# Kernel tuning notes

Measured on AMD Instinct MI355X. Metric: run time of the kernel, lower is better.

The kernel has to match this reference:

```python
import jax, jax.numpy as jnp
import numpy as np

B, T, C = 4, 2048, 1024
H = 16
D = C // H  # head_dim = 64


def setup_inputs() -> dict:
    key = jax.random.key(0)
    ks = jax.random.split(key, 5)
    scale_in = 1.0 / np.sqrt(C)
    x = jax.random.normal(ks[0], (B, T, C), dtype=jnp.float32)
    w_qkv = jax.random.normal(ks[1], (C, 3 * C), dtype=jnp.float32) * scale_in
    b_qkv = jnp.zeros((3 * C,), dtype=jnp.float32)
    w_proj = jax.random.normal(ks[2], (C, C), dtype=jnp.float32) * scale_in
    b_proj = jnp.zeros((C,), dtype=jnp.float32)
    return {"x": x, "w_qkv": w_qkv, "b_qkv": b_qkv, "w_proj": w_proj, "b_proj": b_proj}


def reference(x, w_qkv, b_qkv, w_proj, b_proj):
    # fused QKV projection: [B,T,3C]
    qkv = x @ w_qkv + b_qkv
    q, k, v = jnp.split(qkv, 3, axis=-1)
    # [B,T,C] -> [B,H,T,D]
    q = q.reshape(B, T, H, D).transpose(0, 2, 1, 3)
    k = k.reshape(B, T, H, D).transpose(0, 2, 1, 3)
    v = v.reshape(B, T, H, D).transpose(0, 2, 1, 3)
    scale = 1.0 / np.sqrt(D)
    scores = jnp.einsum('bhqd,bhkd->bhqk', q, k) * scale  # [B,H,T,T]
    causal = jnp.tril(jnp.ones((T, T), dtype=bool))
    scores = jnp.where(causal, scores, jnp.finfo(scores.dtype).min)
    attn = jax.nn.softmax(scores, axis=-1)
    y = jnp.einsum('bhqk,bhkd->bhqd', attn, v)  # [B,H,T,D]
    y = y.transpose(0, 2, 1, 3).reshape(B, T, C)
    return y @ w_proj + b_proj
```

## Files before the change

kernel.cpp:

```cpp
#include <hip/hip_runtime.h>

typedef unsigned short u16;
typedef unsigned int u32;
typedef unsigned long long u64;
typedef __attribute__((ext_vector_type(8))) short s16x8;
typedef __attribute__((ext_vector_type(4))) float f32x4;

#if __has_builtin(__builtin_amdgcn_exp2f)
#define EXP2(x) __builtin_amdgcn_exp2f(x)
#else
#define EXP2(x) __expf((x) * 0.69314718f)
#endif

#if __has_builtin(__builtin_amdgcn_rcpf)
#define RCP(x) __builtin_amdgcn_rcpf(x)
#else
#define RCP(x) (1.0f / (x))
#endif

#define GLL(gp, lp) __builtin_amdgcn_global_load_lds(                         \
    (const __attribute__((address_space(1))) unsigned int*)(const void*)(gp), \
    (__attribute__((address_space(3))) unsigned int*)(void*)(lp), 16, 0, 0)

__device__ __forceinline__ u16 f2bf(float f) {
    union { float f; u32 u; } v; v.f = f;
    u32 r = v.u + 0x7FFF + ((v.u >> 16) & 1);
    return (u16)(r >> 16);
}

__device__ __forceinline__ float bf2f(u16 b) {
    union { u32 u; float f; } v; v.u = ((u32)b) << 16;
    return v.f;
}

__device__ __forceinline__ s16x8 scale_frag(s16x8 v, float s) {
    s16x8 o;
#pragma unroll
    for (int i = 0; i < 8; i++) o[i] = (short)f2bf(bf2f((u16)v[i]) * s);
    return o;
}

__global__ __launch_bounds__(256) void cast_f32_bf16(const float* __restrict__ in,
                                                     u16* __restrict__ out) {
    size_t i = ((size_t)blockIdx.x * 256 + threadIdx.x) * 4;
    float4 f = *(const float4*)(in + i);
    u16 o[4] = { f2bf(f.x), f2bf(f.y), f2bf(f.z), f2bf(f.w) };
    *(unsigned long long*)(out + i) =
        (unsigned long long)o[0] | ((unsigned long long)o[1] << 16) |
        ((unsigned long long)o[2] << 32) | ((unsigned long long)o[3] << 48);
}

__global__ __launch_bounds__(256) void transpose_cast(const float* __restrict__ in,
                                                      u16* __restrict__ out,
                                                      int rows, int cols) {
    __shared__ float tile[32][33];
    int c0 = blockIdx.x * 32, r0 = blockIdx.y * 32;
    int tx = threadIdx.x, ty = threadIdx.y;
    for (int i = 0; i < 32; i += 8)
        tile[ty + i][tx] = in[(size_t)(r0 + ty + i) * cols + (c0 + tx)];
    __syncthreads();
    for (int i = 0; i < 32; i += 8)
        out[(size_t)(c0 + ty + i) * rows + (r0 + tx)] = f2bf(tile[tx][ty + i]);
}

template<int MODE>
__global__ __launch_bounds__(256, 3) void gemm_bt64(const u16* __restrict__ A,
                                                    const u16* __restrict__ BT,
                                                    const float* __restrict__ bias,
                                                    void* __restrict__ O1,
                                                    u16* __restrict__ vT,
                                                    int M, int N, int K) {
    __shared__ u16 As[128 * 64];
    __shared__ u16 Bs[128 * 64];
    int n0 = blockIdx.x * 128, m0 = blockIdx.y * 128;
    int tid = threadIdx.x, lane = tid & 63, w = tid >> 6;
    int row16 = lane & 15, quad = lane >> 4;
    int wm = (w >> 1) * 64, wn = (w & 1) * 64;
    f32x4 acc[4][4] = {};

    int lr = lane >> 3;
    int cswz = (lane & 7) ^ lr;
    const u16* Ag = A + (size_t)(m0 + w * 32 + lr) * K + cswz * 8;
    const u16* Bg = BT + (size_t)(n0 + w * 32 + lr) * K + cswz * 8;
    u16* Asl = As + (w * 32) * 64;
    u16* Bsl = Bs + (w * 32) * 64;

    for (int k0 = 0; k0 < K; k0 += 64) {
        __syncthreads();
#pragma unroll
        for (int j = 0; j < 4; j++) {
            GLL(Ag + k0 + (size_t)j * 8 * K, Asl + j * 8 * 64);
            GLL(Bg + k0 + (size_t)j * 8 * K, Bsl + j * 8 * 64);
        }
        __syncthreads();
#pragma unroll
        for (int kk = 0; kk < 2; kk++) {
            s16x8 af[4], bf[4];
#pragma unroll
            for (int mi = 0; mi < 4; mi++)
                af[mi] = *(const s16x8*)&As[(wm + mi * 16 + row16) * 64 +
                                            (((kk * 4 + quad) ^ (row16 & 7)) * 8)];
#pragma unroll
            for (int ni = 0; ni < 4; ni++)
                bf[ni] = *(const s16x8*)&Bs[(wn + ni * 16 + row16) * 64 +
                                            (((kk * 4 + quad) ^ (row16 & 7)) * 8)];
#pragma unroll
            for (int mi = 0; mi < 4; mi++)
#pragma unroll
                for (int ni = 0; ni < 4; ni++)
                    acc[mi][ni] = __builtin_amdgcn_mfma_f32_16x16x32_bf16(
                        af[mi], bf[ni], acc[mi][ni], 0, 0, 0);
        }
    }

#pragma unroll
    for (int ni = 0; ni < 4; ni++) {
        int col = n0 + wn + ni * 16 + row16;
        float bv = bias[col];
        if (MODE == 0) {
            float* O = (float*)O1;
#pragma unroll
            for (int mi = 0; mi < 4; mi++)
#pragma unroll
                for (int r = 0; r < 4; r++)
                    O[(size_t)(m0 + wm + mi * 16 + quad * 4 + r) * N + col] =
                        acc[mi][ni][r] + bv;
        } else {
            if (col < 2048) {
                u16* qk = (u16*)O1;
#pragma unroll
                for (int mi = 0; mi < 4; mi++)
#pragma unroll
                    for (int r = 0; r < 4; r++)
                        qk[(size_t)(m0 + wm + mi * 16 + quad * 4 + r) * 2048 + col] =
                            f2bf(acc[mi][ni][r] + bv);
            } else {
                int c = col - 2048;
#pragma unroll
                for (int mi = 0; mi < 4; mi++) {
                    int t0 = m0 + wm + mi * 16 + quad * 4;
                    int b = t0 >> 11;
                    u16 o0 = f2bf(acc[mi][ni][0] + bv);
                    u16 o1 = f2bf(acc[mi][ni][1] + bv);
                    u16 o2 = f2bf(acc[mi][ni][2] + bv);
                    u16 o3 = f2bf(acc[mi][ni][3] + bv);
                    u64 pack = (u64)o0 | ((u64)o1 << 16) | ((u64)o2 << 32) | ((u64)o3 << 48);
                    *(u64*)&vT[((size_t)(b * 1024) + c) * 2048 + (t0 & 2047)] = pack;
                }
            }
        }
    }
}

__global__ __launch_bounds__(256, 4) void attn_kernel(const u16* __restrict__ qk,
                                                      const u16* __restrict__ vT,
                                                      u16* __restrict__ y) {
    __shared__ u16 Kb[2][64 * 64];
    __shared__ u16 Vb[2][64 * 64];
    __shared__ u16 Ps[4 * 16 * 64];

    int tid = threadIdx.x, lane = tid & 63, w = tid >> 6;
    int row16 = lane & 15, quad = lane >> 4;
    int pairi = blockIdx.x;
    int bh = blockIdx.y;
    int b = bh >> 4, h = bh & 15;
    const u16* qkb = qk + (size_t)b * 2048 * 2048;
    const u16* vtb = vT + ((size_t)(b * 1024) + h * 64) * 2048;

    int lr = lane >> 3, cswz = (lane & 7) ^ lr;
    const u16* Kg = qkb + (size_t)(w * 16 + lr) * 2048 + 1024 + h * 64 + cswz * 8;
    const u16* Vg = vtb + (size_t)(w * 16 + lr) * 2048 + cswz * 8;
    u16* Psw = Ps + w * 1024;
    int sw = row16 & 7;

    s16x8 ones;
#pragma unroll
    for (int i = 0; i < 8; i++) ones[i] = (short)0x3F80;
    const float qs = 0.125f * 1.44269504f;

    for (int half = 0; half < 2; half++) {
        int qt = half ? pairi : (31 - pairi);
        int q0 = qt * 64;
        int niter = qt + 1;

        int qrow = q0 + w * 16 + row16;
        const u16* qp = qkb + (size_t)qrow * 2048 + h * 64 + quad * 8;
        s16x8 qf0 = scale_frag(*(const s16x8*)qp, qs);
        s16x8 qf1 = scale_frag(*(const s16x8*)(qp + 32), qs);

        f32x4 acc_o[4] = {};
        f32x4 acc_l = {};

        __syncthreads();
#pragma unroll
        for (int j = 0; j < 2; j++) {
            GLL(Kg + (size_t)j * 8 * 2048, Kb[0] + w * 16 * 64 + j * 8 * 64);
            GLL(Vg + (size_t)j * 8 * 2048, Vb[0] + w * 16 * 64 + j * 8 * 64);
        }

        for (int kb = 0; kb < niter; kb++) {
            int cur = kb & 1;
            __syncthreads();
            if (kb + 1 < niter) {
                int k1 = (kb + 1) * 64;
#pragma unroll
                for (int j = 0; j < 2; j++) {
                    GLL(Kg + (size_t)(k1 + j * 8) * 2048, Kb[cur ^ 1] + w * 16 * 64 + j * 8 * 64);
                    GLL(Vg + k1 + (size_t)j * 8 * 2048, Vb[cur ^ 1] + w * 16 * 64 + j * 8 * 64);
                }
            }
            const u16* Kc = Kb[cur];
            const u16* Vc = Vb[cur];
            int k0 = kb * 64;

            f32x4 s[4];
#pragma unroll
            for (int nk = 0; nk < 4; nk++) {
                s16x8 kf0 = *(const s16x8*)&Kc[(nk * 16 + row16) * 64 + ((quad ^ sw) * 8)];
                s16x8 kf1 = *(const s16x8*)&Kc[(nk * 16 + row16) * 64 + (((4 + quad) ^ sw) * 8)];
                f32x4 z = {};
                z = __builtin_amdgcn_mfma_f32_16x16x32_bf16(qf0, kf0, z, 0, 0, 0);
                z = __builtin_amdgcn_mfma_f32_16x16x32_bf16(qf1, kf1, z, 0, 0, 0);
                s[nk] = z;
            }
            if (kb == niter - 1) {
                int rowb = q0 + w * 16 + quad * 4;
#pragma unroll
                for (int nk = 0; nk < 4; nk++) {
                    int kj = k0 + nk * 16 + row16;
#pragma unroll
                    for (int r = 0; r < 4; r++)
                        if (kj > rowb + r) s[nk][r] = -__builtin_inff();
                }
            }
#pragma unroll
            for (int nk = 0; nk < 4; nk++)
#pragma unroll
                for (int r = 0; r < 4; r++) {
                    float p = EXP2(s[nk][r]);
                    int qr = quad * 4 + r;
                    Psw[qr * 64 + (((nk * 2 + (row16 >> 3)) ^ (qr & 7)) * 8) + (row16 & 7)] =
                        f2bf(p);
                }
#pragma unroll
            for (int kk = 0; kk < 2; kk++) {
                s16x8 pf = *(const s16x8*)&Psw[row16 * 64 + (((kk * 4 + quad) ^ sw) * 8)];
#pragma unroll
                for (int nd = 0; nd < 4; nd++) {
                    s16x8 vf = *(const s16x8*)&Vc[(nd * 16 + row16) * 64 +
                                                  (((kk * 4 + quad) ^ sw) * 8)];
                    acc_o[nd] = __builtin_amdgcn_mfma_f32_16x16x32_bf16(pf, vf, acc_o[nd], 0, 0, 0);
                }
                acc_l = __builtin_amdgcn_mfma_f32_16x16x32_bf16(pf, ones, acc_l, 0, 0, 0);
            }
        }

        int t0 = q0 + w * 16 + quad * 4;
#pragma unroll
        for (int r = 0; r < 4; r++) {
            float inv = RCP(acc_l[r]);
#pragma unroll
            for (int nd = 0; nd < 4; nd++)
                y[((size_t)b * 2048 + t0 + r) * 1024 + h * 64 + nd * 16 + row16] =
                    f2bf(acc_o[nd][r] * inv);
        }
    }
}

extern "C" void kernel_launch(void* const* d_in, const int* in_sizes, int n_in,
                              void* d_out, int out_size, void* d_ws, size_t ws_size,
                              hipStream_t stream) {
    const float* x      = (const float*)d_in[0];
    const float* w_qkv  = (const float*)d_in[1];
    const float* b_qkv  = (const float*)d_in[2];
    const float* w_proj = (const float*)d_in[3];
    const float* b_proj = (const float*)d_in[4];
    float* out = (float*)d_out;

    u16* ws     = (u16*)d_ws;
    u16* x_bf   = ws;
    u16* wqkvT  = x_bf  + (size_t)8192 * 1024;
    u16* wprojT = wqkvT + (size_t)3072 * 1024;
    u16* qkbuf  = wprojT + (size_t)1024 * 1024;
    u16* vT     = qkbuf + (size_t)8192 * 2048;
    u16* ybf    = vT    + (size_t)4096 * 2048;

    cast_f32_bf16<<<dim3(8192), dim3(256), 0, stream>>>(x, x_bf);
    transpose_cast<<<dim3(96, 32), dim3(32, 8), 0, stream>>>(w_qkv, wqkvT, 1024, 3072);
    transpose_cast<<<dim3(32, 32), dim3(32, 8), 0, stream>>>(w_proj, wprojT, 1024, 1024);
    gemm_bt64<1><<<dim3(24, 64), 256, 0, stream>>>(x_bf, wqkvT, b_qkv, (void*)qkbuf, vT, 8192, 3072, 1024);
    attn_kernel<<<dim3(16, 64), 256, 0, stream>>>(qkbuf, vT, ybf);
    gemm_bt64<0><<<dim3(8, 64), 256, 0, stream>>>(ybf, wprojT, b_proj, (void*)out, nullptr, 8192, 1024, 1024);
}
```

Measured before the change: 262.7 us.

## Stage V-transpose epilogue through LDS, remap attention blocks per XCD, truncate P

```diff
diff --git a/kernel.cpp b/kernel.cpp
--- a/kernel.cpp
+++ b/kernel.cpp
@@ -26,6 +26,11 @@
     union { float f; u32 u; } v; v.f = f;
     u32 r = v.u + 0x7FFF + ((v.u >> 16) & 1);
     return (u16)(r >> 16);
+}
+
+__device__ __forceinline__ u16 f2bf_trunc(float f) {
+    union { float f; u32 u; } v; v.f = f;
+    return (u16)(v.u >> 16);
 }
 
 __device__ __forceinline__ float bf2f(u16 b) {
@@ -64,14 +69,15 @@
 }
 
 template<int MODE>
-__global__ __launch_bounds__(256, 3) void gemm_bt64(const u16* __restrict__ A,
+__global__ __launch_bounds__(256, 4) void gemm_bt64(const u16* __restrict__ A,
                                                     const u16* __restrict__ BT,
                                                     const float* __restrict__ bias,
                                                     void* __restrict__ O1,
                                                     u16* __restrict__ vT,
                                                     int M, int N, int K) {
-    __shared__ u16 As[128 * 64];
-    __shared__ u16 Bs[128 * 64];
+    __shared__ u16 SMEM[18432];
+    u16* As = SMEM;
+    u16* Bs = SMEM + 8192;
     int n0 = blockIdx.x * 128, m0 = blockIdx.y * 128;
     int tid = threadIdx.x, lane = tid & 63, w = tid >> 6;
     int row16 = lane & 15, quad = lane >> 4;
@@ -113,41 +119,53 @@
         }
     }
 
-#pragma unroll
-    for (int ni = 0; ni < 4; ni++) {
-        int col = n0 + wn + ni * 16 + row16;
-        float bv = bias[col];
-        if (MODE == 0) {
-            float* O = (float*)O1;
+    if (MODE == 0) {
+        float* O = (float*)O1;
+#pragma unroll
+        for (int ni = 0; ni < 4; ni++) {
+            int col = n0 + wn + ni * 16 + row16;
+            float bv = bias[col];
 #pragma unroll
             for (int mi = 0; mi < 4; mi++)
 #pragma unroll
                 for (int r = 0; r < 4; r++)
                     O[(size_t)(m0 + wm + mi * 16 + quad * 4 + r) * N + col] =
                         acc[mi][ni][r] + bv;
-        } else {
-            if (col < 2048) {
-                u16* qk = (u16*)O1;
-#pragma unroll
-                for (int mi = 0; mi < 4; mi++)
-#pragma unroll
-                    for (int r = 0; r < 4; r++)
-                        qk[(size_t)(m0 + wm + mi * 16 + quad * 4 + r) * 2048 + col] =
-                            f2bf(acc[mi][ni][r] + bv);
-            } else {
-                int c = col - 2048;
-#pragma unroll
-                for (int mi = 0; mi < 4; mi++) {
-                    int t0 = m0 + wm + mi * 16 + quad * 4;
-                    int b = t0 >> 11;
-                    u16 o0 = f2bf(acc[mi][ni][0] + bv);
-                    u16 o1 = f2bf(acc[mi][ni][1] + bv);
-                    u16 o2 = f2bf(acc[mi][ni][2] + bv);
-                    u16 o3 = f2bf(acc[mi][ni][3] + bv);
-                    u64 pack = (u64)o0 | ((u64)o1 << 16) | ((u64)o2 << 32) | ((u64)o3 << 48);
-                    *(u64*)&vT[((size_t)(b * 1024) + c) * 2048 + (t0 & 2047)] = pack;
-                }
-            }
+        }
+    } else if (n0 < 2048) {
+        u16* qk = (u16*)O1;
+#pragma unroll
+        for (int ni = 0; ni < 4; ni++) {
+            int col = n0 + wn + ni * 16 + row16;
+            float bv = bias[col];
+#pragma unroll
+            for (int mi = 0; mi < 4; mi++)
+#pragma unroll
+                for (int r = 0; r < 4; r++)
+                    qk[(size_t)(m0 + wm + mi * 16 + quad * 4 + r) * 2048 + col] =
+                        f2bf(acc[mi][ni][r] + bv);
+        }
+    } else {
+        __syncthreads();
+        u16* scr = SMEM + w * 64 * 72;
+#pragma unroll
+        for (int ni = 0; ni < 4; ni++) {
+            float bv = bias[n0 + wn + ni * 16 + row16];
+#pragma unroll
+            for (int mi = 0; mi < 4; mi++)
+#pragma unroll
+                for (int r = 0; r < 4; r++)
+                    scr[(ni * 16 + row16) * 72 + (mi * 16 + quad * 4 + r)] =
+                        f2bf(acc[mi][ni][r] + bv);
+        }
+        __syncthreads();
+        int r8 = lane >> 3, c8 = lane & 7;
+        int vbase = (m0 >> 11) * 1024 + (n0 - 2048) + wn;
+        int tb = (m0 & 2047) + wm;
+#pragma unroll
+        for (int it = 0; it < 8; it++) {
+            s16x8 vv = *(const s16x8*)&scr[(it * 8 + r8) * 72 + c8 * 8];
+            *(s16x8*)&vT[(size_t)(vbase + it * 8 + r8) * 2048 + tb + c8 * 8] = vv;
         }
     }
 }
@@ -161,8 +179,10 @@
 
     int tid = threadIdx.x, lane = tid & 63, w = tid >> 6;
     int row16 = lane & 15, quad = lane >> 4;
-    int pairi = blockIdx.x;
-    int bh = blockIdx.y;
+    int id = blockIdx.x;
+    int xcd = id & 7, slot = id >> 3;
+    int pairi = slot >> 3;
+    int bh = ((slot & 7) << 3) | xcd;
     int b = bh >> 4, h = bh & 15;
     const u16* qkb = qk + (size_t)b * 2048 * 2048;
     const u16* vtb = vT + ((size_t)(b * 1024) + h * 64) * 2048;
@@ -240,7 +260,7 @@
                     float p = EXP2(s[nk][r]);
                     int qr = quad * 4 + r;
                     Psw[qr * 64 + (((nk * 2 + (row16 >> 3)) ^ (qr & 7)) * 8) + (row16 & 7)] =
-                        f2bf(p);
+                        f2bf_trunc(p);
                 }
 #pragma unroll
             for (int kk = 0; kk < 2; kk++) {
@@ -289,6 +309,6 @@
     transpose_cast<<<dim3(96, 32), dim3(32, 8), 0, stream>>>(w_qkv, wqkvT, 1024, 3072);
     transpose_cast<<<dim3(32, 32), dim3(32, 8), 0, stream>>>(w_proj, wprojT, 1024, 1024);
     gemm_bt64<1><<<dim3(24, 64), 256, 0, stream>>>(x_bf, wqkvT, b_qkv, (void*)qkbuf, vT, 8192, 3072, 1024);
-    attn_kernel<<<dim3(16, 64), 256, 0, stream>>>(qkbuf, vT, ybf);
+    attn_kernel<<<dim3(1024), 256, 0, stream>>>(qkbuf, vT, ybf);
     gemm_bt64<0><<<dim3(8, 64), 256, 0, stream>>>(ybf, wprojT, b_proj, (void*)out, nullptr, 8192, 1024, 1024);
 }
```

New measurement: 233.5 us. 1.12x faster.
